# Kernel optimization log

Hardware: AMD Instinct MI355X
Metric: run time of the kernel (lower is better)

## Reference

```python
import jax, jax.numpy as jnp
import numpy as np

PRE_NMS_TOPK = 12000
POST_NMS_TOPK = 1000
NMS_THRESH = 0.7
MIN_SIZE = 1.0
ROI_OUT = 7
ROI_PAD = 6  # max bin extent: ceil(bin)+1 with bin<=26/7 -> <=6


def _gen_anchors(Hf, Wf, stride):
    sizes = jnp.array([128.0, 256.0, 512.0], dtype=jnp.float32)
    ratios = jnp.array([0.5, 1.0, 2.0], dtype=jnp.float32)
    h_r = jnp.sqrt(ratios)
    w_r = 1.0 / h_r
    ws = (w_r[:, None] * sizes[None, :]).reshape(-1)
    hs = (h_r[:, None] * sizes[None, :]).reshape(-1)
    base = jnp.round(jnp.stack([-ws, -hs, ws, hs], axis=1) / 2.0)  # [9,4]
    sx = jnp.arange(Wf, dtype=jnp.float32) * stride
    sy = jnp.arange(Hf, dtype=jnp.float32) * stride
    yy, xx = jnp.meshgrid(sy, sx, indexing='ij')
    shifts = jnp.stack([xx.ravel(), yy.ravel(), xx.ravel(), yy.ravel()], axis=1)
    return (shifts[:, None, :] + base[None, :, :]).reshape(-1, 4)  # [Hf*Wf*9,4]


def _decode(deltas, anchors):
    ax = (anchors[:, 0] + anchors[:, 2]) * 0.5
    ay = (anchors[:, 1] + anchors[:, 3]) * 0.5
    aw = jnp.maximum(anchors[:, 2] - anchors[:, 0], 1e-6)
    ah = jnp.maximum(anchors[:, 3] - anchors[:, 1], 1e-6)
    tx, ty, tw, th = deltas[:, 0], deltas[:, 1], deltas[:, 2], deltas[:, 3]
    px = tx * aw + ax
    py = ty * ah + ay
    pw = aw * jnp.minimum(jnp.exp(tw), 1e6)
    ph = ah * jnp.minimum(jnp.exp(th), 1e6)
    return jnp.stack([px - 0.5 * pw, py - 0.5 * ph, px + 0.5 * pw, py + 0.5 * ph], axis=1)


def _nms(boxes, scores, thresh, max_out):
    x1, y1, x2, y2 = boxes[:, 0], boxes[:, 1], boxes[:, 2], boxes[:, 3]
    areas = (x2 - x1) * (y2 - y1)
    NEG = -jnp.inf
    def body(i, carry):
        s, keep, kv = carry
        j = jnp.argmax(s)
        valid = s[j] > NEG
        iw = jnp.maximum(jnp.minimum(x2, boxes[j, 2]) - jnp.maximum(x1, boxes[j, 0]), 0.0)
        ih = jnp.maximum(jnp.minimum(y2, boxes[j, 3]) - jnp.maximum(y1, boxes[j, 1]), 0.0)
        inter = iw * ih
        iou = inter / jnp.maximum(areas + areas[j] - inter, 1e-12)
        s = jnp.where(iou > thresh, NEG, s).at[j].set(NEG)
        keep = keep.at[i].set(jnp.where(valid, j, 0).astype(jnp.int32))
        kv = kv.at[i].set(valid)
        return (s, keep, kv)
    init = (scores, jnp.zeros((max_out,), jnp.int32), jnp.zeros((max_out,), bool))
    _, keep, kv = jax.lax.fori_loop(0, max_out, body, init)
    return keep, kv


def _rpn_single(cls_i, reg_i, anchors, H, W):
    # cls_i [2A,Hf,Wf], reg_i [4A,Hf,Wf]
    cls2 = jnp.transpose(cls_i, (1, 2, 0)).reshape(-1, 2)
    reg2 = jnp.transpose(reg_i, (1, 2, 0)).reshape(-1, 4)
    probs = jax.nn.softmax(cls2, axis=1)[:, 1]
    K = min(PRE_NMS_TOPK, probs.shape[0])
    scores, idx = jax.lax.top_k(probs, K)
    boxes = _decode(reg2[idx], anchors[idx])
    bx = jnp.clip(boxes[:, 0::2], 0.0, W - 1.0)
    by = jnp.clip(boxes[:, 1::2], 0.0, H - 1.0)
    boxes = jnp.stack([bx[:, 0], by[:, 0], bx[:, 1], by[:, 1]], axis=1)
    ws = jnp.maximum(boxes[:, 2] - boxes[:, 0], 0.0)
    hs = jnp.maximum(boxes[:, 3] - boxes[:, 1], 0.0)
    ok = (ws >= MIN_SIZE) & (hs >= MIN_SIZE)
    scores = jnp.where(ok, scores, -jnp.inf)
    keep, kv = _nms(jax.lax.stop_gradient(boxes), jax.lax.stop_gradient(scores), NMS_THRESH, POST_NMS_TOPK)
    props = boxes[keep] * kv[:, None].astype(boxes.dtype)
    return props, kv


def _roi_pool(feat, boxes, scale):
    # feat [C,Hf,Wf]; boxes [R,4]; exact torchvision roi_pool (max) semantics
    C, Hf, Wf = feat.shape
    x1 = jnp.round(boxes[:, 0] * scale).astype(jnp.int32)
    y1 = jnp.round(boxes[:, 1] * scale).astype(jnp.int32)
    x2 = jnp.round(boxes[:, 2] * scale).astype(jnp.int32)
    y2 = jnp.round(boxes[:, 3] * scale).astype(jnp.int32)
    roi_w = jnp.maximum(x2 - x1 + 1, 1).astype(jnp.float32)
    roi_h = jnp.maximum(y2 - y1 + 1, 1).astype(jnp.float32)
    bw = roi_w / ROI_OUT
    bh = roi_h / ROI_OUT
    j = jnp.arange(ROI_OUT, dtype=jnp.float32)
    wstart = jnp.clip(jnp.floor(j[None, :] * bw[:, None]).astype(jnp.int32) + x1[:, None], 0, Wf)
    wend = jnp.clip(jnp.ceil((j[None, :] + 1) * bw[:, None]).astype(jnp.int32) + x1[:, None], 0, Wf)
    hstart = jnp.clip(jnp.floor(j[None, :] * bh[:, None]).astype(jnp.int32) + y1[:, None], 0, Hf)
    hend = jnp.clip(jnp.ceil((j[None, :] + 1) * bh[:, None]).astype(jnp.int32) + y1[:, None], 0, Hf)
    NEG = -jnp.inf
    R = boxes.shape[0]
    rowpool = jnp.full((R, ROI_OUT, C, Wf), NEG, dtype=feat.dtype)
    for dh in range(ROI_PAD):
        hcur = hstart + dh  # [R,7]
        v = hcur < hend
        g = jnp.take(feat, jnp.clip(hcur, 0, Hf - 1), axis=1)  # [C,R,7,Wf]
        g = jnp.transpose(g, (1, 2, 0, 3))  # [R,7,C,Wf]
        rowpool = jnp.maximum(rowpool, jnp.where(v[:, :, None, None], g, NEG))
    pooled = jnp.full((R, ROI_OUT, C, ROI_OUT), NEG, dtype=feat.dtype)
    def gw(rp_r, wi_r):
        return rp_r[:, :, wi_r]  # [7i,C,7j]
    for dw in range(ROI_PAD):
        wcur = wstart + dw
        v = wcur < wend
        g = jax.vmap(gw)(rowpool, jnp.clip(wcur, 0, Wf - 1))  # [R,7,C,7]
        pooled = jnp.maximum(pooled, jnp.where(v[:, None, None, :], g, NEG))
    pooled = jnp.where(jnp.isneginf(pooled), jnp.zeros((), feat.dtype), pooled)
    return jnp.transpose(pooled, (0, 2, 1, 3))  # [R,C,7,7]


def _model(features, conv_w, conv_b, cls_w, cls_b, reg_w, reg_b, fc1_w, fc1_b,
           fc2_w, fc2_b, cls_score_w, cls_score_b, bbox_w, bbox_b, H, W):
    dn = ('NCHW', 'OIHW', 'NCHW')
    x = jax.lax.conv_general_dilated(features, conv_w, (1, 1), 'SAME', dimension_numbers=dn)
    x = jax.nn.relu(x + conv_b[None, :, None, None])
    cls = jax.lax.conv_general_dilated(x, cls_w, (1, 1), 'SAME', dimension_numbers=dn) + cls_b[None, :, None, None]
    reg = jax.lax.conv_general_dilated(x, reg_w, (1, 1), 'SAME', dimension_numbers=dn) + reg_b[None, :, None, None]
    N, C, Hf, Wf = features.shape
    stride = W // Wf
    anchors = _gen_anchors(Hf, Wf, float(stride))
    props_l, kv_l, pooled_l = [], [], []
    for i in range(N):  # small static batch
        props, kv = _rpn_single(cls[i], reg[i], anchors, float(H), float(W))
        pooled = _roi_pool(features[i], props, 1.0 / stride)
        pooled = pooled * kv[:, None, None, None].astype(features.dtype)
        props_l.append(props); kv_l.append(kv); pooled_l.append(pooled)
    proposals = jnp.stack(props_l)  # [N,1000,4]
    valid = jnp.stack(kv_l)         # [N,1000]
    feats = jnp.concatenate(pooled_l, axis=0).reshape(N * POST_NMS_TOPK, -1)  # [NR, 25088]
    h1 = feats @ fc1_w.T + fc1_b
    h2 = h1 @ fc2_w.T + fc2_b
    logits = h2 @ cls_score_w.T + cls_score_b
    deltas = h2 @ bbox_w.T + bbox_b
    return proposals, valid, logits, deltas


def setup_inputs() -> dict:
    key = jax.random.key(0)
    ks = jax.random.split(key, 10)
    f32 = jnp.float32
    d = {}
    d['features'] = jax.random.normal(ks[0], (1, 512, 25, 25), f32)
    d['conv_w'] = jax.random.normal(ks[1], (512, 512, 3, 3), f32) * 0.02
    d['conv_b'] = jnp.zeros((512,), f32)
    d['cls_w'] = jax.random.normal(ks[2], (18, 512, 1, 1), f32) * 0.02
    d['cls_b'] = jnp.zeros((18,), f32)
    d['reg_w'] = jax.random.normal(ks[3], (36, 512, 1, 1), f32) * 0.01
    d['reg_b'] = jnp.zeros((36,), f32)
    d['fc1_w'] = jax.random.normal(ks[4], (4096, 512 * 7 * 7), f32) * 0.01
    d['fc1_b'] = jnp.zeros((4096,), f32)
    d['fc2_w'] = jax.random.normal(ks[5], (4096, 4096), f32) * 0.01
    d['fc2_b'] = jnp.zeros((4096,), f32)
    d['cls_score_w'] = jax.random.normal(ks[6], (21, 4096), f32) * 0.01
    d['cls_score_b'] = jnp.zeros((21,), f32)
    d['bbox_w'] = jax.random.normal(ks[7], (4, 4096), f32) * 0.01
    d['bbox_b'] = jnp.zeros((4,), f32)
    d['H'] = 800
    d['W'] = 800
    return d


def reference(features, conv_w, conv_b, cls_w, cls_b, reg_w, reg_b, fc1_w, fc1_b,
              fc2_w, fc2_b, cls_score_w, cls_score_b, bbox_w, bbox_b, H, W):
    return _model(features, conv_w, conv_b, cls_w, cls_b, reg_w, reg_b, fc1_w, fc1_b,
                  fc2_w, fc2_b, cls_score_w, cls_score_b, bbox_w, bbox_b, H, W)
```

## Files before the change

kernel.cpp:

```cpp
#include <hip/hip_runtime.h>
#include <math.h>

#define NEGINF (-INFINITY)
#define NBOX 5625
#define NW 88
#define SORTN 8192

typedef __attribute__((ext_vector_type(8))) short short8;
typedef __attribute__((ext_vector_type(4))) float floatx4;

__device__ __forceinline__ unsigned short f2bf(float f) {
  unsigned u = __float_as_uint(f);
  u += 0x7fffu + ((u >> 16) & 1u);
  return (unsigned short)(u >> 16);
}

__device__ __forceinline__ void gload16(const void* g, void* l) {
  __builtin_amdgcn_global_load_lds(
      (const __attribute__((address_space(1))) void*)g,
      (__attribute__((address_space(3))) void*)l, 16, 0, 0);
}

__device__ __forceinline__ unsigned long long shfl_u64(unsigned long long v, int lane) {
  int lo = __shfl((int)(unsigned)v, lane);
  int hi = __shfl((int)(unsigned)(v >> 32), lane);
  return ((unsigned long long)(unsigned)hi << 32) | (unsigned)lo;
}

__global__ __launch_bounds__(128) void conv3x3_relu(
    const float* __restrict__ feat, const float* __restrict__ w,
    const float* __restrict__ bias, float* __restrict__ xt) {
  const int ocg = blockIdx.x;
  const int pg  = blockIdx.y;
  const int t = threadIdx.x;
  const int lr = t / 25, lc = t % 25;
  const bool active = t < 125;
  const int h = pg * 5 + lr;
  __shared__ float sp[7][25];
  float acc[8];
#pragma unroll
  for (int o = 0; o < 8; o++) acc[o] = 0.f;
  const int r0 = pg * 5 - 1;
  for (int ic = 0; ic < 512; ++ic) {
    __syncthreads();
    for (int idx = t; idx < 175; idx += 128) {
      int rr = idx / 25, cc = idx % 25;
      int gr = r0 + rr;
      sp[rr][cc] = (gr >= 0 && gr < 25) ? feat[ic * 625 + gr * 25 + cc] : 0.f;
    }
    __syncthreads();
    if (active) {
      float v[9];
#pragma unroll
      for (int dy = 0; dy < 3; dy++) {
        v[dy * 3 + 0] = (lc > 0)  ? sp[lr + dy][lc - 1] : 0.f;
        v[dy * 3 + 1] = sp[lr + dy][lc];
        v[dy * 3 + 2] = (lc < 24) ? sp[lr + dy][lc + 1] : 0.f;
      }
      const float* wp = w + ((size_t)(ocg * 8) * 512 + ic) * 9;
#pragma unroll
      for (int o = 0; o < 8; o++) {
        const float* wo = wp + (size_t)o * 512 * 9;
        float s = acc[o];
#pragma unroll
        for (int k = 0; k < 9; k++) s = fmaf(v[k], wo[k], s);
        acc[o] = s;
      }
    }
  }
  if (active) {
    int p = h * 25 + lc;
#pragma unroll
    for (int o = 0; o < 8; o++) {
      int oc = ocg * 8 + o;
      xt[(size_t)p * 512 + oc] = fmaxf(acc[o] + bias[oc], 0.f);
    }
  }
}

__global__ void conv1x1_kernel(const float* __restrict__ xt,
    const float* __restrict__ cls_w, const float* __restrict__ cls_b,
    const float* __restrict__ reg_w, const float* __restrict__ reg_b,
    float* __restrict__ out) {
  int gid = blockIdx.x * blockDim.x + threadIdx.x;
  int p = gid >> 6, c = gid & 63;
  if (p >= 625 || c >= 54) return;
  const float* wrow;
  float b;
  if (c < 18) { wrow = cls_w + (size_t)c * 512; b = cls_b[c]; }
  else        { wrow = reg_w + (size_t)(c - 18) * 512; b = reg_b[c - 18]; }
  const float* xr = xt + (size_t)p * 512;
  float s = 0.f;
  for (int k = 0; k < 512; k++) s = fmaf(xr[k], wrow[k], s);
  out[p * 54 + c] = s + b;
}

__global__ void decode_kernel(const float* __restrict__ clsreg,
    const int* __restrict__ Hp, const int* __restrict__ Wp,
    float* __restrict__ boxes, float* __restrict__ areas, float* __restrict__ scores) {
  int n = blockIdx.x * blockDim.x + threadIdx.x;
  if (n >= NBOX) return;
  int p = n / 9, a = n % 9;
  int hh = p / 25, ww = p % 25;
  float Wlim = (float)(*Wp), Hlim = (float)(*Hp);
  float stride = (float)((*Wp) / 25);
  int ri = a / 3, si = a % 3;
  float ratio = (ri == 0) ? 0.5f : ((ri == 1) ? 1.0f : 2.0f);
  float size  = (si == 0) ? 128.f : ((si == 1) ? 256.f : 512.f);
  float hr = sqrtf(ratio);
  float wr = 1.0f / hr;
  float wsz = wr * size, hsz = hr * size;
  float bx1 = rintf(-wsz * 0.5f), by1 = rintf(-hsz * 0.5f);
  float bx2 = rintf( wsz * 0.5f), by2 = rintf( hsz * 0.5f);
  float sx = (float)ww * stride, sy = (float)hh * stride;
  float a0 = sx + bx1, a1 = sy + by1, a2 = sx + bx2, a3 = sy + by2;
  float ax = (a0 + a2) * 0.5f, ay = (a1 + a3) * 0.5f;
  float aw = fmaxf(a2 - a0, 1e-6f), ah = fmaxf(a3 - a1, 1e-6f);
  const float* row = clsreg + p * 54;
  float c0 = row[a * 2], c1 = row[a * 2 + 1];
  float m = fmaxf(c0, c1);
  float e0 = expf(c0 - m), e1 = expf(c1 - m);
  float prob = e1 / (e0 + e1);
  float tx = row[18 + a * 4 + 0], ty = row[18 + a * 4 + 1];
  float tw = row[18 + a * 4 + 2], th = row[18 + a * 4 + 3];
  float px = tx * aw + ax, py = ty * ah + ay;
  float pw = aw * fminf(expf(tw), 1e6f);
  float ph = ah * fminf(expf(th), 1e6f);
  float x1 = px - 0.5f * pw, y1 = py - 0.5f * ph;
  float x2 = px + 0.5f * pw, y2 = py + 0.5f * ph;
  x1 = fminf(fmaxf(x1, 0.f), Wlim - 1.f); x2 = fminf(fmaxf(x2, 0.f), Wlim - 1.f);
  y1 = fminf(fmaxf(y1, 0.f), Hlim - 1.f); y2 = fminf(fmaxf(y2, 0.f), Hlim - 1.f);
  float bw = fmaxf(x2 - x1, 0.f), bh = fmaxf(y2 - y1, 0.f);
  bool ok = (bw >= 1.0f) && (bh >= 1.0f);
  boxes[n * 4 + 0] = x1; boxes[n * 4 + 1] = y1;
  boxes[n * 4 + 2] = x2; boxes[n * 4 + 3] = y2;
  areas[n] = (x2 - x1) * (y2 - y1);
  scores[n] = ok ? prob : NEGINF;
}

__global__ __launch_bounds__(256) void nms_pack(const float* __restrict__ scores,
    unsigned long long* __restrict__ keys) {
  int n = blockIdx.x * 256 + threadIdx.x;
  if (n >= SORTN) return;
  unsigned long long key;
  if (n < NBOX) {
    unsigned u = __float_as_uint(scores[n]);
    u = (u & 0x80000000u) ? ~u : (u | 0x80000000u);
    key = ~(((unsigned long long)u << 32) | (unsigned long long)(0xFFFFFFFFu ^ (unsigned)n));
  } else {
    key = ~0ULL;
  }
  keys[n] = key;
}

__global__ __launch_bounds__(1024) void nms_sort(unsigned long long* __restrict__ keys) {
  __shared__ unsigned long long s[SORTN];
  const int t = threadIdx.x;
  for (int i = t; i < SORTN; i += 1024) s[i] = keys[i];
  __syncthreads();
  for (int k = 2; k <= SORTN; k <<= 1) {
    for (int j = k >> 1; j > 0; j >>= 1) {
      for (int i = t; i < SORTN; i += 1024) {
        int l = i ^ j;
        if (l > i) {
          unsigned long long a = s[i], b = s[l];
          bool up = ((i & k) == 0);
          if ((a > b) == up) { s[i] = b; s[l] = a; }
        }
      }
      __syncthreads();
    }
  }
  for (int i = t; i < SORTN; i += 1024) keys[i] = s[i];
}

__global__ __launch_bounds__(64) void nms_unpack(
    const unsigned long long* __restrict__ keys,
    const float* __restrict__ boxes, const float* __restrict__ areas,
    float* __restrict__ sbox, float* __restrict__ sarea,
    unsigned long long* __restrict__ vmask) {
  int i = blockIdx.x * 64 + threadIdx.x;
  unsigned long long k = ~keys[i];
  unsigned up = (unsigned)(k >> 32);
  bool valid = up > 0x007FFFFFu;
  if (valid) {
    unsigned n = 0xFFFFFFFFu ^ (unsigned)k;
    sbox[i * 4 + 0] = boxes[n * 4 + 0];
    sbox[i * 4 + 1] = boxes[n * 4 + 1];
    sbox[i * 4 + 2] = boxes[n * 4 + 2];
    sbox[i * 4 + 3] = boxes[n * 4 + 3];
    sarea[i] = areas[n];
  } else {
    sbox[i * 4 + 0] = 0.f; sbox[i * 4 + 1] = 0.f;
    sbox[i * 4 + 2] = 0.f; sbox[i * 4 + 3] = 0.f;
    sarea[i] = 0.f;
  }
  unsigned long long vb = __ballot(valid);
  if (threadIdx.x == 0) vmask[blockIdx.x] = vb;
}

__global__ __launch_bounds__(64) void nms_mask(
    const float* __restrict__ sbox, const float* __restrict__ sarea,
    unsigned long long* __restrict__ mask) {
  const int cb = blockIdx.x, rb = blockIdx.y;
  const int t = threadIdx.x;
  const int r = rb * 64 + t;
  if (cb < rb) { mask[(size_t)r * NW + cb] = 0ULL; return; }
  __shared__ float cx1[64], cy1[64], cx2[64], cy2[64], car[64];
  int j = cb * 64 + t;
  cx1[t] = sbox[j * 4 + 0]; cy1[t] = sbox[j * 4 + 1];
  cx2[t] = sbox[j * 4 + 2]; cy2[t] = sbox[j * 4 + 3];
  car[t] = sarea[j];
  __syncthreads();
  float rx1 = sbox[r * 4 + 0], ry1 = sbox[r * 4 + 1];
  float rx2 = sbox[r * 4 + 2], ry2 = sbox[r * 4 + 3];
  float rar = sarea[r];
  unsigned long long m = 0;
  int c0 = (cb == rb) ? (t + 1) : 0;
  for (int c = c0; c < 64; ++c) {
    float iw = fmaxf(fminf(rx2, cx2[c]) - fmaxf(rx1, cx1[c]), 0.f);
    float ih = fmaxf(fminf(ry2, cy2[c]) - fmaxf(ry1, cy1[c]), 0.f);
    float inter = iw * ih;
    float iou = inter / fmaxf(rar + car[c] - inter, 1e-12f);
    if (iou > 0.7f) m |= (1ULL << c);
  }
  mask[(size_t)r * NW + cb] = m;
}

__global__ __launch_bounds__(64) void nms_scan(
    const unsigned long long* __restrict__ vmask,
    const unsigned long long* __restrict__ mask,
    const float* __restrict__ sbox, float* __restrict__ dout) {
  float* props  = dout;
  float* validf = dout + 4000;
  const int l = threadIdx.x;
  unsigned long long rem0 = 0, rem1 = 0;
  unsigned long long v0 = vmask[l];
  unsigned long long v1 = (l < 24) ? vmask[64 + l] : 0ULL;
  int kept = 0;
  for (int w = 0; w < NW; ++w) {
    int owner = (w < 64) ? w : (w - 64);
    for (;;) {
      unsigned long long myc = (w < 64) ? (v0 & ~rem0) : (v1 & ~rem1);
      unsigned long long cand = shfl_u64(myc, owner);
      if (!cand) break;
      int b = __ffsll((unsigned long long)cand) - 1;
      int i = w * 64 + b;
      if (l < 4) props[kept * 4 + l] = sbox[(size_t)i * 4 + l];
      if (l == 0) validf[kept] = 1.0f;
      kept++;
      if (kept == 1000) { w = NW; break; }
      unsigned long long m0 = mask[(size_t)i * NW + l];
      unsigned long long m1 = (l < 24) ? mask[(size_t)i * NW + 64 + l] : 0ULL;
      rem0 |= m0; rem1 |= m1;
      if (w < 64) { if (l == w) rem0 |= (1ULL << b); }
      else        { if (l == w - 64) rem1 |= (1ULL << b); }
    }
  }
  for (int z = kept * 4 + l; z < 4000; z += 64) props[z] = 0.f;
  for (int z = kept + l; z < 1000; z += 64) validf[z] = 0.f;
}

__global__ __launch_bounds__(256) void roipool_kernel(
    const float* __restrict__ feat, const float* __restrict__ dout,
    const int* __restrict__ Wp, unsigned short* __restrict__ feats) {
  const int r = blockIdx.x;
  const int t = threadIdx.x;
  const float* props  = dout;
  const float* validf = dout + 4000;
  unsigned short* outr = feats + (size_t)r * 25088;
  bool dead = (r >= 1000) || (validf[r] == 0.0f);
  if (dead) {
    for (int i = t; i < 25088; i += 256) outr[i] = 0;
    return;
  }
  const float scale = 1.0f / (float)((*Wp) / 25);
  __shared__ int hs_[7], he_[7], ws_[7], we_[7];
  if (t < 7) {
    float fx1 = props[r * 4 + 0], fy1 = props[r * 4 + 1];
    float fx2 = props[r * 4 + 2], fy2 = props[r * 4 + 3];
    int x1 = (int)rintf(fx1 * scale), y1 = (int)rintf(fy1 * scale);
    int x2 = (int)rintf(fx2 * scale), y2 = (int)rintf(fy2 * scale);
    float roiw = (float)max(x2 - x1 + 1, 1);
    float roih = (float)max(y2 - y1 + 1, 1);
    float bw = roiw / 7.0f, bh = roih / 7.0f;
    float jf = (float)t;
    int w0 = (int)floorf(jf * bw) + x1;
    int w1 = (int)ceilf((jf + 1.f) * bw) + x1;
    int h0 = (int)floorf(jf * bh) + y1;
    int h1 = (int)ceilf((jf + 1.f) * bh) + y1;
    ws_[t] = min(max(w0, 0), 25); we_[t] = min(max(w1, 0), 25);
    hs_[t] = min(max(h0, 0), 25); he_[t] = min(max(h1, 0), 25);
  }
  __syncthreads();
  for (int idx = t; idx < 25088; idx += 256) {
    int c = idx / 49;
    int ij = idx % 49;
    int i = ij / 7, j = ij % 7;
    int h0 = hs_[i], h1 = min(he_[i], h0 + 6);
    int w0 = ws_[j], w1 = min(we_[j], w0 + 6);
    float m = NEGINF;
    const float* fp = feat + (size_t)c * 625;
    for (int y = h0; y < h1; y++)
      for (int x = w0; x < w1; x++)
        m = fmaxf(m, fp[y * 25 + x]);
    outr[idx] = (h0 < h1 && w0 < w1) ? f2bf(m) : 0;
  }
}

__global__ __launch_bounds__(256) void gemm_bt_bf16(
    const unsigned short* __restrict__ A, int lda,
    const unsigned short* __restrict__ B, int ldb,
    const float* __restrict__ bias, float* __restrict__ C, int ldc,
    int K, int beta) {
  __shared__ unsigned short As[128 * 32];
  __shared__ unsigned short Bs[128 * 32];
  const int t = threadIdx.x;
  const int lane = t & 63;
  const int wv = t >> 6;
  const int wr = wv >> 1, wc = wv & 1;
  const int quad = lane >> 4, l16 = lane & 15;
  const int m0 = blockIdx.x * 128, n0 = blockIdx.y * 128;
  floatx4 acc[4][4];
#pragma unroll
  for (int mi = 0; mi < 4; mi++)
#pragma unroll
    for (int ni = 0; ni < 4; ni++) acc[mi][ni] = (floatx4){0.f, 0.f, 0.f, 0.f};
  const int srow = t >> 2;
  const int scol = (t & 3) * 8;
  const unsigned short* Ag0 = A + (size_t)(m0 + srow) * lda + scol;
  const unsigned short* Ag1 = A + (size_t)(m0 + 64 + srow) * lda + scol;
  const unsigned short* Bg0 = B + (size_t)(n0 + srow) * ldb + scol;
  const unsigned short* Bg1 = B + (size_t)(n0 + 64 + srow) * ldb + scol;
  unsigned short* la0 = As + t * 8;
  unsigned short* la1 = As + 2048 + t * 8;
  unsigned short* lb0 = Bs + t * 8;
  unsigned short* lb1 = Bs + 2048 + t * 8;
  for (int kt = 0; kt < K; kt += 32) {
    __syncthreads();
    gload16(Ag0 + kt, la0);
    gload16(Ag1 + kt, la1);
    gload16(Bg0 + kt, lb0);
    gload16(Bg1 + kt, lb1);
    __syncthreads();
    short8 af[4], bfr[4];
#pragma unroll
    for (int mi = 0; mi < 4; mi++)
      af[mi] = *(const short8*)(As + (wr * 64 + mi * 16 + l16) * 32 + quad * 8);
#pragma unroll
    for (int ni = 0; ni < 4; ni++)
      bfr[ni] = *(const short8*)(Bs + (wc * 64 + ni * 16 + l16) * 32 + quad * 8);
#pragma unroll
    for (int mi = 0; mi < 4; mi++)
#pragma unroll
      for (int ni = 0; ni < 4; ni++)
        acc[mi][ni] = __builtin_amdgcn_mfma_f32_16x16x32_bf16(af[mi], bfr[ni], acc[mi][ni], 0, 0, 0);
  }
#pragma unroll
  for (int mi = 0; mi < 4; mi++) {
#pragma unroll
    for (int ni = 0; ni < 4; ni++) {
      int gn = n0 + wc * 64 + ni * 16 + l16;
      float bv = bias ? bias[gn] : 0.f;
#pragma unroll
      for (int r = 0; r < 4; r++) {
        int gm = m0 + wr * 64 + mi * 16 + quad * 4 + r;
        size_t o = (size_t)gm * ldc + gn;
        float v = acc[mi][ni][r] + bv;
        C[o] = beta ? (C[o] + v) : v;
      }
    }
  }
}

__global__ __launch_bounds__(256) void cvt_fc1_chunk(
    const float* __restrict__ w, unsigned short* __restrict__ o, int koff) {
  int idx = blockIdx.x * 256 + threadIdx.x;
  int e = idx * 4;
  if (e >= 4096 * 6272) return;
  int n = e / 6272, k = e - n * 6272;
  float4 v = *(const float4*)(w + (size_t)n * 25088 + koff + k);
  ushort4 r = make_ushort4(f2bf(v.x), f2bf(v.y), f2bf(v.z), f2bf(v.w));
  *(ushort4*)(o + e) = r;
}

__global__ __launch_bounds__(256) void cvt_f32_bf16(
    const float* __restrict__ in, unsigned short* __restrict__ out, int n4) {
  int idx = blockIdx.x * 256 + threadIdx.x;
  if (idx >= n4) return;
  float4 v = *(const float4*)(in + (size_t)idx * 4);
  ushort4 r = make_ushort4(f2bf(v.x), f2bf(v.y), f2bf(v.z), f2bf(v.w));
  *(ushort4*)(out + (size_t)idx * 4) = r;
}

__global__ __launch_bounds__(256) void cvt_h1(
    const float* __restrict__ h1, const float* __restrict__ b,
    unsigned short* __restrict__ o) {
  int idx = blockIdx.x * 256 + threadIdx.x;
  int e = idx * 4;
  if (e >= 1024 * 4096) return;
  int col = e & 4095;
  float4 v = *(const float4*)(h1 + e);
  float4 bb = *(const float4*)(b + col);
  ushort4 r = make_ushort4(f2bf(v.x + bb.x), f2bf(v.y + bb.y),
                           f2bf(v.z + bb.z), f2bf(v.w + bb.w));
  *(ushort4*)(o + e) = r;
}

__global__ __launch_bounds__(256) void final_fc(
    const float* __restrict__ h2, const float* __restrict__ cw,
    const float* __restrict__ cb, const float* __restrict__ bw,
    const float* __restrict__ bb, float* __restrict__ logits,
    float* __restrict__ deltas) {
  int r = blockIdx.x;
  const float* x = h2 + (size_t)r * 4096;
  int lane = threadIdx.x & 63, w = threadIdx.x >> 6;
  for (int o = w; o < 25; o += 4) {
    const float* wt = (o < 21) ? (cw + (size_t)o * 4096) : (bw + (size_t)(o - 21) * 4096);
    float s = 0.f;
    for (int k = lane; k < 4096; k += 64) s = fmaf(x[k], wt[k], s);
#pragma unroll
    for (int off = 32; off >= 1; off >>= 1) s += __shfl_xor(s, off);
    if (lane == 0) {
      if (o < 21) logits[r * 21 + o] = s + cb[o];
      else        deltas[r * 4 + (o - 21)] = s + bb[o - 21];
    }
  }
}

extern "C" void kernel_launch(void* const* d_in, const int* in_sizes, int n_in,
                              void* d_out, int out_size, void* d_ws, size_t ws_size,
                              hipStream_t stream) {
  const float* features    = (const float*)d_in[0];
  const float* conv_w      = (const float*)d_in[1];
  const float* conv_b      = (const float*)d_in[2];
  const float* cls_w       = (const float*)d_in[3];
  const float* cls_b       = (const float*)d_in[4];
  const float* reg_w       = (const float*)d_in[5];
  const float* reg_b       = (const float*)d_in[6];
  const float* fc1_w       = (const float*)d_in[7];
  const float* fc1_b       = (const float*)d_in[8];
  const float* fc2_w       = (const float*)d_in[9];
  const float* fc2_b       = (const float*)d_in[10];
  const float* cls_score_w = (const float*)d_in[11];
  const float* cls_score_b = (const float*)d_in[12];
  const float* bbox_w      = (const float*)d_in[13];
  const float* bbox_b      = (const float*)d_in[14];
  const int*   Hp          = (const int*)d_in[15];
  const int*   Wp          = (const int*)d_in[16];
  float* out = (float*)d_out;

  char* w8 = (char*)d_ws;
  float* xt     = (float*)w8;
  float* clsreg = xt + 320000;
  float* boxes  = clsreg + 33750;
  float* areas  = boxes + 22500;
  float* scores = areas + 5625;
  unsigned short* feats = (unsigned short*)(w8 + 1550000);
  float* h1f            = (float*)(w8 + 52930224);
  unsigned short* wchunk = (unsigned short*)(w8 + 69707440);
  unsigned short* fc2wb = wchunk;
  unsigned short* h1b   = (unsigned short*)(w8 + 69707440 + 33554432);
  float* h2             = (float*)feats;
  char* nbase = w8 + 1550000;
  unsigned long long* keys  = (unsigned long long*)nbase;
  float* sbox               = (float*)(nbase + 65536);
  float* sarea              = (float*)(nbase + 155648);
  unsigned long long* vmask = (unsigned long long*)(nbase + 178176);
  unsigned long long* mask  = (unsigned long long*)(nbase + 178880);

  conv3x3_relu<<<dim3(64, 5), 128, 0, stream>>>(features, conv_w, conv_b, xt);
  conv1x1_kernel<<<dim3(157), 256, 0, stream>>>(xt, cls_w, cls_b, reg_w, reg_b, clsreg);
  decode_kernel<<<dim3(23), 256, 0, stream>>>(clsreg, Hp, Wp, boxes, areas, scores);

  nms_pack<<<dim3(SORTN / 256), 256, 0, stream>>>(scores, keys);
  nms_sort<<<dim3(1), 1024, 0, stream>>>(keys);
  nms_unpack<<<dim3(NW), 64, 0, stream>>>(keys, boxes, areas, sbox, sarea, vmask);
  nms_mask<<<dim3(NW, NW), 64, 0, stream>>>(sbox, sarea, mask);
  nms_scan<<<dim3(1), 64, 0, stream>>>(vmask, mask, sbox, out);

  roipool_kernel<<<dim3(1024), 256, 0, stream>>>(features, out, Wp, feats);

  for (int kc = 0; kc < 4; kc++) {
    cvt_fc1_chunk<<<dim3(25088), 256, 0, stream>>>(fc1_w, wchunk, kc * 6272);
    gemm_bt_bf16<<<dim3(8, 32), 256, 0, stream>>>(
        feats + kc * 6272, 25088, wchunk, 6272, nullptr, h1f, 4096, 6272, kc > 0 ? 1 : 0);
  }
  cvt_h1<<<dim3(4096), 256, 0, stream>>>(h1f, fc1_b, h1b);

  cvt_f32_bf16<<<dim3(16384), 256, 0, stream>>>(fc2_w, fc2wb, 4194304);
  gemm_bt_bf16<<<dim3(8, 32), 256, 0, stream>>>(
      h1b, 4096, fc2wb, 4096, fc2_b, h2, 4096, 4096, 0);

  final_fc<<<dim3(1000), 256, 0, stream>>>(h2, cls_score_w, cls_score_b,
                                           bbox_w, bbox_b, out + 5000, out + 26000);
}
```

Measured before the change: 3.299 ms.

## Transpose conv weights and split 3x3 conv into more blocks with two outputs

```diff
diff --git a/kernel.cpp b/kernel.cpp
--- a/kernel.cpp
+++ b/kernel.cpp
@@ -27,55 +27,61 @@
   return ((unsigned long long)(unsigned)hi << 32) | (unsigned)lo;
 }
 
-__global__ __launch_bounds__(128) void conv3x3_relu(
-    const float* __restrict__ feat, const float* __restrict__ w,
+__global__ __launch_bounds__(256) void wtrans_kernel(
+    const float* __restrict__ w, float* __restrict__ wt) {
+  int e = blockIdx.x * 256 + threadIdx.x;
+  if (e >= 512 * 512 * 9) return;
+  int oc = e / 4608;
+  int rem = e - oc * 4608;
+  int ic = rem / 9;
+  int k = rem - ic * 9;
+  wt[(size_t)ic * 4608 + oc * 9 + k] = w[e];
+}
+
+__global__ __launch_bounds__(128) void conv3x3_o2(
+    const float* __restrict__ feat, const float* __restrict__ wt,
     const float* __restrict__ bias, float* __restrict__ xt) {
-  const int ocg = blockIdx.x;
-  const int pg  = blockIdx.y;
+  const int og = blockIdx.x;
+  const int pg = blockIdx.y;
   const int t = threadIdx.x;
+  if (t >= 125) return;
   const int lr = t / 25, lc = t % 25;
-  const bool active = t < 125;
   const int h = pg * 5 + lr;
-  __shared__ float sp[7][25];
-  float acc[8];
-#pragma unroll
-  for (int o = 0; o < 8; o++) acc[o] = 0.f;
-  const int r0 = pg * 5 - 1;
+  const bool ok_t = (h > 0), ok_b = (h < 24);
+  const bool ok_l = (lc > 0), ok_r = (lc < 24);
+  const float* fbase = feat + h * 25 + lc;
+  int vz;
+  asm volatile("v_mov_b32 %0, 0" : "=v"(vz));
+  const float* wbase = wt + og * 18 + vz;
+  float acc0 = 0.f, acc1 = 0.f;
+#pragma unroll 2
   for (int ic = 0; ic < 512; ++ic) {
-    __syncthreads();
-    for (int idx = t; idx < 175; idx += 128) {
-      int rr = idx / 25, cc = idx % 25;
-      int gr = r0 + rr;
-      sp[rr][cc] = (gr >= 0 && gr < 25) ? feat[ic * 625 + gr * 25 + cc] : 0.f;
-    }
-    __syncthreads();
-    if (active) {
-      float v[9];
-#pragma unroll
-      for (int dy = 0; dy < 3; dy++) {
-        v[dy * 3 + 0] = (lc > 0)  ? sp[lr + dy][lc - 1] : 0.f;
-        v[dy * 3 + 1] = sp[lr + dy][lc];
-        v[dy * 3 + 2] = (lc < 24) ? sp[lr + dy][lc + 1] : 0.f;
-      }
-      const float* wp = w + ((size_t)(ocg * 8) * 512 + ic) * 9;
-#pragma unroll
-      for (int o = 0; o < 8; o++) {
-        const float* wo = wp + (size_t)o * 512 * 9;
-        float s = acc[o];
-#pragma unroll
-        for (int k = 0; k < 9; k++) s = fmaf(v[k], wo[k], s);
-        acc[o] = s;
-      }
-    }
-  }
-  if (active) {
-    int p = h * 25 + lc;
-#pragma unroll
-    for (int o = 0; o < 8; o++) {
-      int oc = ocg * 8 + o;
-      xt[(size_t)p * 512 + oc] = fmaxf(acc[o] + bias[oc], 0.f);
-    }
-  }
+    const float* fp = fbase + (size_t)ic * 625;
+    float v[9];
+    v[0] = (ok_t && ok_l) ? fp[-26] : 0.f;
+    v[1] = ok_t ? fp[-25] : 0.f;
+    v[2] = (ok_t && ok_r) ? fp[-24] : 0.f;
+    v[3] = ok_l ? fp[-1] : 0.f;
+    v[4] = fp[0];
+    v[5] = ok_r ? fp[1] : 0.f;
+    v[6] = (ok_b && ok_l) ? fp[24] : 0.f;
+    v[7] = ok_b ? fp[25] : 0.f;
+    v[8] = (ok_b && ok_r) ? fp[26] : 0.f;
+    float wq[18];
+    const float2* wp2 = (const float2*)(wbase + (size_t)ic * 4608);
+#pragma unroll
+    for (int q = 0; q < 9; q++) *(float2*)(&wq[q * 2]) = wp2[q];
+    float s0 = acc0, s1 = acc1;
+#pragma unroll
+    for (int k = 0; k < 9; k++) s0 = fmaf(v[k], wq[k], s0);
+#pragma unroll
+    for (int k = 0; k < 9; k++) s1 = fmaf(v[k], wq[9 + k], s1);
+    acc0 = s0; acc1 = s1;
+  }
+  const int p = h * 25 + lc;
+  const int oc0 = og * 2;
+  xt[(size_t)p * 512 + oc0]     = fmaxf(acc0 + bias[oc0], 0.f);
+  xt[(size_t)p * 512 + oc0 + 1] = fmaxf(acc1 + bias[oc0 + 1], 0.f);
 }
 
 __global__ void conv1x1_kernel(const float* __restrict__ xt,
@@ -462,6 +468,7 @@
   unsigned short* fc2wb = wchunk;
   unsigned short* h1b   = (unsigned short*)(w8 + 69707440 + 33554432);
   float* h2             = (float*)feats;
+  float* wt_buf = (float*)(w8 + 1550000);
   char* nbase = w8 + 1550000;
   unsigned long long* keys  = (unsigned long long*)nbase;
   float* sbox               = (float*)(nbase + 65536);
@@ -469,7 +476,9 @@
   unsigned long long* vmask = (unsigned long long*)(nbase + 178176);
   unsigned long long* mask  = (unsigned long long*)(nbase + 178880);
 
-  conv3x3_relu<<<dim3(64, 5), 128, 0, stream>>>(features, conv_w, conv_b, xt);
+  wtrans_kernel<<<dim3(9216), 256, 0, stream>>>(conv_w, wt_buf);
+  conv3x3_o2<<<dim3(256, 5), 128, 0, stream>>>(features, wt_buf, conv_b, xt);
+
   conv1x1_kernel<<<dim3(157), 256, 0, stream>>>(xt, cls_w, cls_b, reg_w, reg_b, clsreg);
   decode_kernel<<<dim3(23), 256, 0, stream>>>(clsreg, Hp, Wp, boxes, areas, scores);
 
```

Measured after the change: 3.179 ms. 1.04x faster.
